# Performance work log

Measured on AMD Instinct MI355X. Metric: run time of the kernel, lower is better.

The kernel has to match this reference:

```python
import jax, jax.numpy as jnp
import numpy as np

LREL = 0.01  # LeakyReLU default negative_slope

L, D, B = 256, 64, 32


def setup_inputs() -> dict:
    key = jax.random.key(0)
    ks = jax.random.split(key, 10)
    return {
        "emb": jax.random.normal(ks[0], (B, L * D + 1), jnp.float32),
        "tw": jax.random.normal(ks[1], (L * D + 1,), jnp.float32) * 0.02,
        "tb": jax.random.normal(ks[2], (1,), jnp.float32) * 0.02,
        "w1": jax.random.normal(ks[3], (D, 2 * D), jnp.float32) * (1.0 / np.sqrt(2 * D)),
        "b1": jax.random.normal(ks[4], (D,), jnp.float32) * 0.02,
        "w2": jax.random.normal(ks[5], (16, D), jnp.float32) * (1.0 / np.sqrt(D)),
        "b2": jax.random.normal(ks[6], (16,), jnp.float32) * 0.02,
        "w3": jax.random.normal(ks[7], (1, 16), jnp.float32) * 0.25,
        "b3": jax.random.normal(ks[8], (1,), jnp.float32) * 0.02,
        "scale": jnp.array([0.2], jnp.float32),
    }


def reference(emb, tw, tb, w1, b1, w2, b2, w3, b3, scale):
    # first-order term: Linear(L*D+1 -> 1), squeezed
    x1 = emb @ tw + tb[0]  # [B]

    x2 = emb[:, :-1].reshape(emb.shape[0], L, D)  # [B,L,D]
    mask = (jnp.abs(x2).sum(-1) > 0).astype(emb.dtype)  # [B,L]
    pmask = mask[:, :, None] * mask[:, None, :]  # [B,L,L]

    w = tw[:-1].reshape(1, L, D)
    x2 = x2 * w

    xi = x2[:, :, None, :]  # [B,L,1,D]
    xj = x2[:, None, :, :]  # [B,1,L,D]
    feat = jnp.concatenate(
        [jnp.broadcast_to((xi + xj) * 0.5, (emb.shape[0], L, L, D)),
         jnp.broadcast_to(jnp.abs(xi - xj), (emb.shape[0], L, L, D))],
        axis=-1)  # [B,L,L,2D]

    h = jax.nn.leaky_relu(jnp.einsum('bijf,df->bijd', feat, w1) + b1, LREL)
    h = jax.nn.leaky_relu(jnp.einsum('bijd,kd->bijk', h, w2) + b2, LREL)
    s = (jnp.einsum('bijk,ok->bijo', h, w3) + b3)[..., 0]  # [B,L,L]

    s = s * pmask
    s = jnp.triu(s, k=1).sum(axis=(1, 2)) * scale[0]  # [B]
    return x1 + s
```

## Files before the change

kernel.cpp:

```cpp
#include <hip/hip_runtime.h>

typedef _Float16 half8 __attribute__((ext_vector_type(8)));
typedef _Float16 half2v __attribute__((ext_vector_type(2)));
typedef short    s16x8 __attribute__((ext_vector_type(8)));
typedef float    f32x4 __attribute__((ext_vector_type(4)));

#define LL 256
#define DD 64
#define BB 32
#define LREL 0.01f
#define EMBC (LL*DD + 1)

__global__ void k_prep(const float* __restrict__ emb, const float* __restrict__ tw,
                       _Float16* __restrict__ y16, float* __restrict__ maskw)
{
    int lin  = blockIdx.x * 4 + (threadIdx.x >> 6);
    int lane = threadIdx.x & 63;
    int b = lin >> 8, l = lin & 255;
    float e = emb[(size_t)b * EMBC + l * 64 + lane];
    float t = tw[l * 64 + lane];
    y16[((size_t)(b * 256 + l)) * 64 + lane] = (_Float16)(e * t);
    float a = fabsf(e);
    #pragma unroll
    for (int m = 32; m; m >>= 1) a += __shfl_xor(a, m, 64);
    if (lane == 0) maskw[b * 256 + l] = (a > 0.f) ? 1.f : 0.f;
}

__global__ void k_prepw(const float* __restrict__ w1, const float* __restrict__ w2,
                        _Float16* __restrict__ w1h, _Float16* __restrict__ w2h)
{
    int idx = blockIdx.x * 256 + threadIdx.x;
    if (idx < 8192)       w1h[idx] = (_Float16)w1[idx];
    else if (idx < 9216)  w2h[idx - 8192] = (_Float16)w2[idx - 8192];
}

__global__ void k_x1(const float* __restrict__ emb, const float* __restrict__ tw,
                     const float* __restrict__ tb, float* __restrict__ x1ws,
                     float* __restrict__ bsum)
{
    int b = blockIdx.x, tid = threadIdx.x;
    const float* row = emb + (size_t)b * EMBC;
    float part = 0.f;
    for (int c = tid; c < EMBC; c += 256) part = fmaf(row[c], tw[c], part);
    __shared__ float red[256];
    red[tid] = part; __syncthreads();
    for (int s = 128; s; s >>= 1) { if (tid < s) red[tid] += red[tid + s]; __syncthreads(); }
    if (tid == 0) { x1ws[b] = red[0] + tb[0]; bsum[b] = 0.f; }
}

__global__ __launch_bounds__(256, 2) void k_main(
    const _Float16* __restrict__ y16, const float* __restrict__ maskw,
    const _Float16* __restrict__ w1h, const _Float16* __restrict__ w2h,
    const float* __restrict__ b1, const float* __restrict__ b2,
    const float* __restrict__ w3, const float* __restrict__ b3,
    float* __restrict__ bsum)
{
    const int tid = threadIdx.x;
    const int lane = tid & 63, wid = tid >> 6;
    const int g = lane >> 4, p = lane & 15;

    int blk = blockIdx.x;
    int batch = blk / 40;
    int t = blk % 40;
    int bi, bj;
    if (t < 4)       { bj = 0; bi = t; }
    else if (t < 12) { bj = 1; bi = t - 4; }
    else if (t < 24) { bj = 2; bi = t - 12; }
    else             { bj = 3; bi = t - 24; }
    const int i0 = bi * 16, j0 = bj * 64;

    __shared__ _Float16 yi_s[16][72];
    __shared__ _Float16 yj_s[64][72];
    __shared__ _Float16 h1_s[4][16][72];
    __shared__ float mi_s[16];
    __shared__ float mj_s[64];

    const _Float16* ybase = y16 + (size_t)batch * (LL * DD);
    for (int r = tid; r < 80 * 8; r += 256) {
        int row = r >> 3, c = r & 7;
        if (row < 16)
            *(float4*)&yi_s[row][c * 8] = *(const float4*)(ybase + (i0 + row) * 64 + c * 8);
        else {
            int rr = row - 16;
            *(float4*)&yj_s[rr][c * 8] = *(const float4*)(ybase + (j0 + rr) * 64 + c * 8);
        }
    }
    if (tid < 16) mi_s[tid] = maskw[batch * LL + i0 + tid];
    if (tid < 64) mj_s[tid] = maskw[batch * LL + j0 + tid];
    __syncthreads();

    half8 w1f[4][4];
    #pragma unroll
    for (int T = 0; T < 4; ++T)
        #pragma unroll
        for (int kb = 0; kb < 4; ++kb)
            w1f[T][kb] = *(const half8*)(w1h + (T * 16 + p) * 128 + kb * 32 + g * 8);
    half8 w2f[2];
    #pragma unroll
    for (int kb = 0; kb < 2; ++kb)
        w2f[kb] = *(const half8*)(w2h + p * 64 + kb * 32 + g * 8);

    f32x4 b1v[4];
    #pragma unroll
    for (int T = 0; T < 4; ++T) b1v[T] = *(const f32x4*)(b1 + T * 16 + g * 4);
    f32x4 b2v = *(const f32x4*)(b2 + g * 4);
    f32x4 w3v = *(const f32x4*)(w3 + g * 4);
    const float b3v = (g == 0) ? b3[0] : 0.f;

    const int jl = wid * 16 + p;
    const int jglob = j0 + jl;
    const float mj = mj_s[jl];
    const half8 yjA = *(const half8*)&yj_s[jl][g * 8];
    const half8 yjB = *(const half8*)&yj_s[jl][32 + g * 8];
    const int jmax = j0 + wid * 16 + 15;

    float sacc = 0.f;
    const _Float16 h05 = (_Float16)0.5f;

    for (int il = 0; il < 16; ++il) {
        const int i = i0 + il;
        if (jmax <= i) continue;

        const half8 yiA = *(const half8*)&yi_s[il][g * 8];
        const half8 yiB = *(const half8*)&yi_s[il][32 + g * 8];

        half8 f0 = (yiA + yjA) * h05;
        half8 f1 = (yiB + yjB) * h05;
        s16x8 ad0 = __builtin_bit_cast(s16x8, yiA - yjA) & (short)0x7FFF;
        s16x8 ad1 = __builtin_bit_cast(s16x8, yiB - yjB) & (short)0x7FFF;
        half8 f2 = __builtin_bit_cast(half8, ad0);
        half8 f3 = __builtin_bit_cast(half8, ad1);

        f32x4 acc[4] = {};
        #pragma unroll
        for (int T = 0; T < 4; ++T) {
            acc[T] = __builtin_amdgcn_mfma_f32_16x16x32_f16(w1f[T][0], f0, acc[T], 0, 0, 0);
            acc[T] = __builtin_amdgcn_mfma_f32_16x16x32_f16(w1f[T][1], f1, acc[T], 0, 0, 0);
            acc[T] = __builtin_amdgcn_mfma_f32_16x16x32_f16(w1f[T][2], f2, acc[T], 0, 0, 0);
            acc[T] = __builtin_amdgcn_mfma_f32_16x16x32_f16(w1f[T][3], f3, acc[T], 0, 0, 0);
        }

        #pragma unroll
        for (int T = 0; T < 4; ++T) {
            float h0 = acc[T][0] + b1v[T][0];
            float h1 = acc[T][1] + b1v[T][1];
            float h2 = acc[T][2] + b1v[T][2];
            float h3 = acc[T][3] + b1v[T][3];
            h0 = fmaxf(h0, 0.f) + LREL * fminf(h0, 0.f);
            h1 = fmaxf(h1, 0.f) + LREL * fminf(h1, 0.f);
            h2 = fmaxf(h2, 0.f) + LREL * fminf(h2, 0.f);
            h3 = fmaxf(h3, 0.f) + LREL * fminf(h3, 0.f);
            half2v p01, p23;
            p01[0] = (_Float16)h0; p01[1] = (_Float16)h1;
            p23[0] = (_Float16)h2; p23[1] = (_Float16)h3;
            *(half2v*)&h1_s[wid][p][T * 16 + g * 4]     = p01;
            *(half2v*)&h1_s[wid][p][T * 16 + g * 4 + 2] = p23;
        }

        const half8 hB0 = *(const half8*)&h1_s[wid][p][g * 8];
        const half8 hB1 = *(const half8*)&h1_s[wid][p][32 + g * 8];
        f32x4 acc2 = {};
        acc2 = __builtin_amdgcn_mfma_f32_16x16x32_f16(w2f[0], hB0, acc2, 0, 0, 0);
        acc2 = __builtin_amdgcn_mfma_f32_16x16x32_f16(w2f[1], hB1, acc2, 0, 0, 0);

        float sp = b3v;
        #pragma unroll
        for (int r = 0; r < 4; ++r) {
            float h = acc2[r] + b2v[r];
            h = fmaxf(h, 0.f) + LREL * fminf(h, 0.f);
            sp += h * w3v[r];
        }
        const float mfac = (jglob > i) ? (mi_s[il] * mj) : 0.f;
        sacc += sp * mfac;
    }

    #pragma unroll
    for (int m = 32; m; m >>= 1) sacc += __shfl_xor(sacc, m, 64);
    if (lane == 0) atomicAdd(&bsum[batch], sacc);
}

__global__ void k_fin(const float* __restrict__ x1ws, const float* __restrict__ bsum,
                      const float* __restrict__ scale, float* __restrict__ out)
{
    int t = threadIdx.x;
    if (t < BB) out[t] = x1ws[t] + bsum[t] * scale[0];
}

extern "C" void kernel_launch(void* const* d_in, const int* in_sizes, int n_in,
                              void* d_out, int out_size, void* d_ws, size_t ws_size,
                              hipStream_t stream)
{
    const float* emb   = (const float*)d_in[0];
    const float* tw    = (const float*)d_in[1];
    const float* tb    = (const float*)d_in[2];
    const float* w1    = (const float*)d_in[3];
    const float* b1    = (const float*)d_in[4];
    const float* w2    = (const float*)d_in[5];
    const float* b2    = (const float*)d_in[6];
    const float* w3    = (const float*)d_in[7];
    const float* b3    = (const float*)d_in[8];
    const float* scale = (const float*)d_in[9];

    char* ws = (char*)d_ws;
    _Float16* y16 = (_Float16*)(ws + 0);
    float*    maskw = (float*)(ws + 1048576);
    _Float16* w1h  = (_Float16*)(ws + 1081344);
    _Float16* w2h  = (_Float16*)(ws + 1097728);
    float*    x1ws = (float*)(ws + 1099776);
    float*    bsum = (float*)(ws + 1099904);
    float*    out  = (float*)d_out;

    hipLaunchKernelGGL(k_prep,  dim3(2048), dim3(256), 0, stream, emb, tw, y16, maskw);
    hipLaunchKernelGGL(k_prepw, dim3(36),   dim3(256), 0, stream, w1, w2, w1h, w2h);
    hipLaunchKernelGGL(k_x1,    dim3(32),   dim3(256), 0, stream, emb, tw, tb, x1ws, bsum);
    hipLaunchKernelGGL(k_main,  dim3(1280), dim3(256), 0, stream, y16, maskw, w1h, w2h,
                       b1, b2, w3, b3, bsum);
    hipLaunchKernelGGL(k_fin,   dim3(1),    dim3(64),  0, stream, x1ws, bsum, scale, out);
}
```

Baseline: 156.0 us.

## Fuse prep kernels, shrink main tiles, fold bias/scale, finalize via last-block atomic

```diff
diff --git a/kernel.cpp b/kernel.cpp
--- a/kernel.cpp
+++ b/kernel.cpp
@@ -1,92 +1,98 @@
 #include <hip/hip_runtime.h>
 
-typedef _Float16 half8 __attribute__((ext_vector_type(8)));
+typedef _Float16 half8  __attribute__((ext_vector_type(8)));
 typedef _Float16 half2v __attribute__((ext_vector_type(2)));
-typedef short    s16x8 __attribute__((ext_vector_type(8)));
-typedef float    f32x4 __attribute__((ext_vector_type(4)));
+typedef short    s16x8  __attribute__((ext_vector_type(8)));
+typedef float    f32x4  __attribute__((ext_vector_type(4)));
 
 #define LL 256
 #define DD 64
 #define BB 32
 #define LREL 0.01f
 #define EMBC (LL*DD + 1)
-
-__global__ void k_prep(const float* __restrict__ emb, const float* __restrict__ tw,
-                       _Float16* __restrict__ y16, float* __restrict__ maskw)
+#define NTILE 72
+#define NBLK_MAIN (BB * NTILE)
+
+__global__ void k_prep_all(const float* __restrict__ emb, const float* __restrict__ tw,
+                           const float* __restrict__ w1, const float* __restrict__ w2,
+                           _Float16* __restrict__ y16, float* __restrict__ maskw,
+                           _Float16* __restrict__ w1h, _Float16* __restrict__ w2h,
+                           float* __restrict__ x1part, float* __restrict__ bc)
 {
-    int lin  = blockIdx.x * 4 + (threadIdx.x >> 6);
-    int lane = threadIdx.x & 63;
-    int b = lin >> 8, l = lin & 255;
-    float e = emb[(size_t)b * EMBC + l * 64 + lane];
-    float t = tw[l * 64 + lane];
-    y16[((size_t)(b * 256 + l)) * 64 + lane] = (_Float16)(e * t);
-    float a = fabsf(e);
-    #pragma unroll
-    for (int m = 32; m; m >>= 1) a += __shfl_xor(a, m, 64);
-    if (lane == 0) maskw[b * 256 + l] = (a > 0.f) ? 1.f : 0.f;
+    int blk = blockIdx.x, tid = threadIdx.x;
+    if (blk < 2048) {
+        int lin = blk * 4 + (tid >> 6);
+        int lane = tid & 63;
+        int b = lin >> 8, l = lin & 255;
+        float e = emb[(size_t)b * EMBC + l * 64 + lane];
+        float t = tw[l * 64 + lane];
+        y16[((size_t)(b * 256 + l)) * 64 + lane] = (_Float16)(e * t * 0.5f);
+        float a = fabsf(e);
+        #pragma unroll
+        for (int m = 32; m; m >>= 1) a += __shfl_xor(a, m, 64);
+        if (lane == 0) maskw[b * 256 + l] = (a > 0.f) ? 1.f : 0.f;
+    } else if (blk < 2084) {
+        int idx = (blk - 2048) * 256 + tid;
+        if (idx < 8192) {
+            float v = w1[idx];
+            if ((idx & 127) >= 64) v *= 2.f;
+            w1h[idx] = (_Float16)v;
+        } else if (idx < 9216) {
+            w2h[idx - 8192] = (_Float16)w2[idx - 8192];
+        }
+        if (blk == 2048 && tid < 33) bc[tid] = 0.f;
+    } else {
+        int bl = blk - 2084;
+        int b = bl >> 2, q = bl & 3;
+        const float* row = emb + (size_t)b * EMBC;
+        int cend = (q + 1) * 4097; if (cend > EMBC) cend = EMBC;
+        float part = 0.f;
+        for (int c = q * 4097 + tid; c < cend; c += 256) part = fmaf(row[c], tw[c], part);
+        __shared__ float red[256];
+        red[tid] = part; __syncthreads();
+        for (int s = 128; s; s >>= 1) { if (tid < s) red[tid] += red[tid + s]; __syncthreads(); }
+        if (tid == 0) x1part[bl] = red[0];
+    }
 }
 
-__global__ void k_prepw(const float* __restrict__ w1, const float* __restrict__ w2,
-                        _Float16* __restrict__ w1h, _Float16* __restrict__ w2h)
-{
-    int idx = blockIdx.x * 256 + threadIdx.x;
-    if (idx < 8192)       w1h[idx] = (_Float16)w1[idx];
-    else if (idx < 9216)  w2h[idx - 8192] = (_Float16)w2[idx - 8192];
-}
-
-__global__ void k_x1(const float* __restrict__ emb, const float* __restrict__ tw,
-                     const float* __restrict__ tb, float* __restrict__ x1ws,
-                     float* __restrict__ bsum)
-{
-    int b = blockIdx.x, tid = threadIdx.x;
-    const float* row = emb + (size_t)b * EMBC;
-    float part = 0.f;
-    for (int c = tid; c < EMBC; c += 256) part = fmaf(row[c], tw[c], part);
-    __shared__ float red[256];
-    red[tid] = part; __syncthreads();
-    for (int s = 128; s; s >>= 1) { if (tid < s) red[tid] += red[tid + s]; __syncthreads(); }
-    if (tid == 0) { x1ws[b] = red[0] + tb[0]; bsum[b] = 0.f; }
-}
-
-__global__ __launch_bounds__(256, 2) void k_main(
+__global__ __launch_bounds__(128) void k_main(
     const _Float16* __restrict__ y16, const float* __restrict__ maskw,
     const _Float16* __restrict__ w1h, const _Float16* __restrict__ w2h,
     const float* __restrict__ b1, const float* __restrict__ b2,
     const float* __restrict__ w3, const float* __restrict__ b3,
-    float* __restrict__ bsum)
+    const float* __restrict__ x1part, const float* __restrict__ tb,
+    const float* __restrict__ scale, float* __restrict__ bc,
+    float* __restrict__ out)
 {
     const int tid = threadIdx.x;
     const int lane = tid & 63, wid = tid >> 6;
     const int g = lane >> 4, p = lane & 15;
 
-    int blk = blockIdx.x;
-    int batch = blk / 40;
-    int t = blk % 40;
-    int bi, bj;
-    if (t < 4)       { bj = 0; bi = t; }
-    else if (t < 12) { bj = 1; bi = t - 4; }
-    else if (t < 24) { bj = 2; bi = t - 12; }
-    else             { bj = 3; bi = t - 24; }
-    const int i0 = bi * 16, j0 = bj * 64;
+    const int blk = blockIdx.x;
+    const int batch = blk / NTILE;
+    const int t = blk - batch * NTILE;
+    int bj, bi;
+    if (t < 12)      { if (t < 2) { bj = 0; bi = t; } else if (t < 6) { bj = 1; bi = t - 2; } else { bj = 2; bi = t - 6; } }
+    else if (t < 30) { if (t < 20) { bj = 3; bi = t - 12; } else { bj = 4; bi = t - 20; } }
+    else             { if (t < 42) { bj = 5; bi = t - 30; } else if (t < 56) { bj = 6; bi = t - 42; } else { bj = 7; bi = t - 56; } }
+    const int i0 = bi * 16, j0 = bj * 32;
 
     __shared__ _Float16 yi_s[16][72];
-    __shared__ _Float16 yj_s[64][72];
-    __shared__ _Float16 h1_s[4][16][72];
-    __shared__ float mi_s[16];
-    __shared__ float mj_s[64];
+    __shared__ _Float16 yj_s[32][72];
+    __shared__ _Float16 h1_s[2][16][72];
+    __shared__ float mi_s[16], mj_s[32];
+    __shared__ int lastflag;
 
     const _Float16* ybase = y16 + (size_t)batch * (LL * DD);
-    for (int r = tid; r < 80 * 8; r += 256) {
+    for (int r = tid; r < 48 * 8; r += 128) {
         int row = r >> 3, c = r & 7;
-        if (row < 16)
-            *(float4*)&yi_s[row][c * 8] = *(const float4*)(ybase + (i0 + row) * 64 + c * 8);
-        else {
-            int rr = row - 16;
-            *(float4*)&yj_s[rr][c * 8] = *(const float4*)(ybase + (j0 + rr) * 64 + c * 8);
-        }
-    }
-    if (tid < 16) mi_s[tid] = maskw[batch * LL + i0 + tid];
-    if (tid < 64) mj_s[tid] = maskw[batch * LL + j0 + tid];
+        int pos = (row < 16) ? (i0 + row) : (j0 + row - 16);
+        float4 v = *(const float4*)(ybase + pos * 64 + c * 8);
+        if (row < 16) *(float4*)&yi_s[row][c * 8] = v;
+        else          *(float4*)&yj_s[row - 16][c * 8] = v;
+    }
+    if (tid < 16)      mi_s[tid]      = maskw[batch * LL + i0 + tid];
+    else if (tid < 48) mj_s[tid - 16] = maskw[batch * LL + j0 + tid - 16];
     __syncthreads();
 
     half8 w1f[4][4];
@@ -103,8 +109,8 @@
     f32x4 b1v[4];
     #pragma unroll
     for (int T = 0; T < 4; ++T) b1v[T] = *(const f32x4*)(b1 + T * 16 + g * 4);
-    f32x4 b2v = *(const f32x4*)(b2 + g * 4);
-    f32x4 w3v = *(const f32x4*)(w3 + g * 4);
+    const f32x4 b2v = *(const f32x4*)(b2 + g * 4);
+    const f32x4 w3v = *(const f32x4*)(w3 + g * 4);
     const float b3v = (g == 0) ? b3[0] : 0.f;
 
     const int jl = wid * 16 + p;
@@ -112,26 +118,27 @@
     const float mj = mj_s[jl];
     const half8 yjA = *(const half8*)&yj_s[jl][g * 8];
     const half8 yjB = *(const half8*)&yj_s[jl][32 + g * 8];
+
     const int jmax = j0 + wid * 16 + 15;
+    int nil = jmax - i0; if (nil > 16) nil = 16;
+
+    const half2v lrel2 = {(_Float16)LREL, (_Float16)LREL};
+    const half2v zero2 = {};
 
     float sacc = 0.f;
-    const _Float16 h05 = (_Float16)0.5f;
-
-    for (int il = 0; il < 16; ++il) {
+    for (int il = 0; il < nil; ++il) {
         const int i = i0 + il;
-        if (jmax <= i) continue;
-
         const half8 yiA = *(const half8*)&yi_s[il][g * 8];
         const half8 yiB = *(const half8*)&yi_s[il][32 + g * 8];
 
-        half8 f0 = (yiA + yjA) * h05;
-        half8 f1 = (yiB + yjB) * h05;
+        half8 f0 = yiA + yjA;
+        half8 f1 = yiB + yjB;
         s16x8 ad0 = __builtin_bit_cast(s16x8, yiA - yjA) & (short)0x7FFF;
         s16x8 ad1 = __builtin_bit_cast(s16x8, yiB - yjB) & (short)0x7FFF;
         half8 f2 = __builtin_bit_cast(half8, ad0);
         half8 f3 = __builtin_bit_cast(half8, ad1);
 
-        f32x4 acc[4] = {};
+        f32x4 acc[4] = {b1v[0], b1v[1], b1v[2], b1v[3]};
         #pragma unroll
         for (int T = 0; T < 4; ++T) {
             acc[T] = __builtin_amdgcn_mfma_f32_16x16x32_f16(w1f[T][0], f0, acc[T], 0, 0, 0);
@@ -142,48 +149,49 @@
 
         #pragma unroll
         for (int T = 0; T < 4; ++T) {
-            float h0 = acc[T][0] + b1v[T][0];
-            float h1 = acc[T][1] + b1v[T][1];
-            float h2 = acc[T][2] + b1v[T][2];
-            float h3 = acc[T][3] + b1v[T][3];
-            h0 = fmaxf(h0, 0.f) + LREL * fminf(h0, 0.f);
-            h1 = fmaxf(h1, 0.f) + LREL * fminf(h1, 0.f);
-            h2 = fmaxf(h2, 0.f) + LREL * fminf(h2, 0.f);
-            h3 = fmaxf(h3, 0.f) + LREL * fminf(h3, 0.f);
-            half2v p01, p23;
-            p01[0] = (_Float16)h0; p01[1] = (_Float16)h1;
-            p23[0] = (_Float16)h2; p23[1] = (_Float16)h3;
-            *(half2v*)&h1_s[wid][p][T * 16 + g * 4]     = p01;
-            *(half2v*)&h1_s[wid][p][T * 16 + g * 4 + 2] = p23;
+            half2v a = __builtin_bit_cast(half2v, __builtin_amdgcn_cvt_pkrtz(acc[T][0], acc[T][1]));
+            half2v b = __builtin_bit_cast(half2v, __builtin_amdgcn_cvt_pkrtz(acc[T][2], acc[T][3]));
+            a = __builtin_elementwise_max(a, zero2) + lrel2 * __builtin_elementwise_min(a, zero2);
+            b = __builtin_elementwise_max(b, zero2) + lrel2 * __builtin_elementwise_min(b, zero2);
+            *(unsigned*)&h1_s[wid][p][T * 16 + g * 4]     = __builtin_bit_cast(unsigned, a);
+            *(unsigned*)&h1_s[wid][p][T * 16 + g * 4 + 2] = __builtin_bit_cast(unsigned, b);
         }
 
         const half8 hB0 = *(const half8*)&h1_s[wid][p][g * 8];
         const half8 hB1 = *(const half8*)&h1_s[wid][p][32 + g * 8];
-        f32x4 acc2 = {};
-        acc2 = __builtin_amdgcn_mfma_f32_16x16x32_f16(w2f[0], hB0, acc2, 0, 0, 0);
-        acc2 = __builtin_amdgcn_mfma_f32_16x16x32_f16(w2f[1], hB1, acc2, 0, 0, 0);
+
+        f32x4 a2 = b2v;
+        a2 = __builtin_amdgcn_mfma_f32_16x16x32_f16(w2f[0], hB0, a2, 0, 0, 0);
+        a2 = __builtin_amdgcn_mfma_f32_16x16x32_f16(w2f[1], hB1, a2, 0, 0, 0);
 
         float sp = b3v;
         #pragma unroll
         for (int r = 0; r < 4; ++r) {
-            float h = acc2[r] + b2v[r];
+            float h = a2[r];
             h = fmaxf(h, 0.f) + LREL * fminf(h, 0.f);
-            sp += h * w3v[r];
+            sp = fmaf(h, w3v[r], sp);
         }
         const float mfac = (jglob > i) ? (mi_s[il] * mj) : 0.f;
-        sacc += sp * mfac;
+        sacc = fmaf(sp, mfac, sacc);
     }
 
     #pragma unroll
     for (int m = 32; m; m >>= 1) sacc += __shfl_xor(sacc, m, 64);
-    if (lane == 0) atomicAdd(&bsum[batch], sacc);
-}
-
-__global__ void k_fin(const float* __restrict__ x1ws, const float* __restrict__ bsum,
-                      const float* __restrict__ scale, float* __restrict__ out)
-{
-    int t = threadIdx.x;
-    if (t < BB) out[t] = x1ws[t] + bsum[t] * scale[0];
+    if (lane == 0) atomicAdd(&bc[batch], sacc);
+
+    __syncthreads();
+    if (tid == 0) {
+        __threadfence();
+        float old = atomicAdd(&bc[32], 1.0f);
+        lastflag = (old >= (float)(NBLK_MAIN - 1)) ? 1 : 0;
+    }
+    __syncthreads();
+    if (lastflag && tid < BB) {
+        float bs = atomicAdd(&bc[tid], 0.0f);
+        float x1 = x1part[tid * 4] + x1part[tid * 4 + 1] + x1part[tid * 4 + 2]
+                 + x1part[tid * 4 + 3] + tb[0];
+        out[tid] = fmaf(bs, scale[0], x1);
+    }
 }
 
 extern "C" void kernel_launch(void* const* d_in, const int* in_sizes, int n_in,
@@ -202,18 +210,16 @@
     const float* scale = (const float*)d_in[9];
 
     char* ws = (char*)d_ws;
-    _Float16* y16 = (_Float16*)(ws + 0);
+    _Float16* y16   = (_Float16*)(ws + 0);
     float*    maskw = (float*)(ws + 1048576);
-    _Float16* w1h  = (_Float16*)(ws + 1081344);
-    _Float16* w2h  = (_Float16*)(ws + 1097728);
-    float*    x1ws = (float*)(ws + 1099776);
-    float*    bsum = (float*)(ws + 1099904);
-    float*    out  = (float*)d_out;
-
-    hipLaunchKernelGGL(k_prep,  dim3(2048), dim3(256), 0, stream, emb, tw, y16, maskw);
-    hipLaunchKernelGGL(k_prepw, dim3(36),   dim3(256), 0, stream, w1, w2, w1h, w2h);
-    hipLaunchKernelGGL(k_x1,    dim3(32),   dim3(256), 0, stream, emb, tw, tb, x1ws, bsum);
-    hipLaunchKernelGGL(k_main,  dim3(1280), dim3(256), 0, stream, y16, maskw, w1h, w2h,
-                       b1, b2, w3, b3, bsum);
-    hipLaunchKernelGGL(k_fin,   dim3(1),    dim3(64),  0, stream, x1ws, bsum, scale, out);
+    _Float16* w1h   = (_Float16*)(ws + 1081344);
+    _Float16* w2h   = (_Float16*)(ws + 1097728);
+    float*    x1part= (float*)(ws + 1099776);
+    float*    bc    = (float*)(ws + 1100288);
+    float*    out   = (float*)d_out;
+
+    hipLaunchKernelGGL(k_prep_all, dim3(2048 + 36 + 128), dim3(256), 0, stream,
+                       emb, tw, w1, w2, y16, maskw, w1h, w2h, x1part, bc);
+    hipLaunchKernelGGL(k_main, dim3(NBLK_MAIN), dim3(128), 0, stream,
+                       y16, maskw, w1h, w2h, b1, b2, w3, b3, x1part, tb, scale, bc, out);
 }
```

Result: no change. 154.1 us (-1.2%).
